# Optimization experiments

Measured on AMD Instinct MI355X. Metric: run time of the kernel, lower is better.

Reference implementation:

```python
import jax, jax.numpy as jnp
import numpy as np

B, S, IN, D, H, L, DFF, C = 64, 256, 32, 512, 8, 2, 2048, 16
DH = D // H


def setup_inputs() -> dict:
    key = jax.random.key(0)
    ks = iter(jax.random.split(key, 40))
    r = lambda shp, s=0.02: (jax.random.normal(next(ks), shp, dtype=jnp.float32) * s)
    inp = {
        'x': jax.random.normal(next(ks), (B, S, IN), dtype=jnp.float32),
        'W_emb': r((IN, D)), 'b_emb': jnp.zeros((D,), jnp.float32),
        'Wq': r((L, D, D)), 'bq': jnp.zeros((L, D), jnp.float32),
        'Wk': r((L, D, D)), 'bk': jnp.zeros((L, D), jnp.float32),
        'Wv': r((L, D, D)), 'bv': jnp.zeros((L, D), jnp.float32),
        'Wo': r((L, D, D)), 'bo': jnp.zeros((L, D), jnp.float32),
        'ln1_s': jnp.ones((L, D), jnp.float32), 'ln1_b': jnp.zeros((L, D), jnp.float32),
        'W1': r((L, D, DFF)), 'b1': jnp.zeros((L, DFF), jnp.float32),
        'W2': r((L, DFF, D)), 'b2': jnp.zeros((L, D), jnp.float32),
        'ln2_s': jnp.ones((L, D), jnp.float32), 'ln2_b': jnp.zeros((L, D), jnp.float32),
        'e1_w': r((D, 128)), 'e1_b': jnp.zeros((128,), jnp.float32),
        'e2_w': r((128, D)), 'e2_b': jnp.zeros((D,), jnp.float32),
        'd1_w': r((D, 128)), 'd1_b': jnp.zeros((128,), jnp.float32),
        'd2_w': r((128, D)), 'd2_b': jnp.zeros((D,), jnp.float32),
        'y': jax.random.randint(next(ks), (B, S, 1), 0, C, dtype=jnp.int32),
    }
    return inp


def _ln(x, s, b):
    m = x.mean(-1, keepdims=True)
    v = ((x - m) ** 2).mean(-1, keepdims=True)
    return (x - m) / jnp.sqrt(v + 1e-5) * s + b


def _ari(a, t, n_cls):
    # adjusted rand index from contingency matrix (labels in [0, n_cls))
    idx = a * n_cls + t
    cm = jnp.zeros((n_cls * n_cls,), jnp.float32).at[idx].add(1.0).reshape(n_cls, n_cls)
    comb2 = lambda m: m * (m - 1.0) * 0.5
    sij = comb2(cm).sum()
    sa = comb2(cm.sum(1)).sum()
    sb = comb2(cm.sum(0)).sum()
    n = jnp.float32(a.shape[0])
    exp = sa * sb / (n * (n - 1.0) * 0.5)
    mx = 0.5 * (sa + sb)
    return (sij - exp) / (mx - exp)


def _net(x, W_emb, b_emb, Wq, bq, Wk, bk, Wv, bv, Wo, bo, ln1_s, ln1_b,
         W1, b1, W2, b2, ln2_s, ln2_b, e1_w, e1_b, e2_w, e2_b, d1_w, d1_b, d2_w, d2_b):
    h = x @ W_emb + b_emb  # [B,S,D]
    for l in range(L):
        q = (h @ Wq[l] + bq[l]).reshape(B, S, H, DH)
        k = (h @ Wk[l] + bk[l]).reshape(B, S, H, DH)
        v = (h @ Wv[l] + bv[l]).reshape(B, S, H, DH)
        scores = jnp.einsum('bqhd,bkhd->bhqk', q, k) / jnp.sqrt(jnp.float32(DH))
        attn = jax.nn.softmax(scores, axis=-1)
        o = jnp.einsum('bhqk,bkhd->bqhd', attn, v).reshape(B, S, D)
        h = _ln(h + o @ Wo[l] + bo[l], ln1_s[l], ln1_b[l])
        f = jax.nn.relu(h @ W1[l] + b1[l]) @ W2[l] + b2[l]
        h = _ln(h + f, ln2_s[l], ln2_b[l])
    enc = jax.nn.relu(h @ e1_w + e1_b) @ e2_w + e2_b
    z = jax.nn.relu(enc @ d1_w + d1_b) @ d2_w + d2_b  # input_to_cluster [B,S,D]
    return z


def reference(x, W_emb, b_emb, Wq, bq, Wk, bk, Wv, bv, Wo, bo, ln1_s, ln1_b,
              W1, b1, W2, b2, ln2_s, ln2_b, e1_w, e1_b, e2_w, e2_b,
              d1_w, d1_b, d2_w, d2_b, y):
    z = _net(x, W_emb, b_emb, Wq, bq, Wk, bk, Wv, bv, Wo, bo, ln1_s, ln1_b,
             W1, b1, W2, b2, ln2_s, ln2_b, e1_w, e1_b, e2_w, e2_b, d1_w, d1_b, d2_w, d2_b)
    # pairwise squared distances across batch per timestep: [S,B,B]
    sq = jnp.sum(z * z, -1)                       # [B,S]
    gram = jnp.einsum('bsd,csd->sbc', z, z)       # [S,B,B]
    dist = sq.T[:, :, None] + sq.T[:, None, :] - 2.0 * gram
    p = jax.nn.softmax(-dist, axis=-1)
    _, knn = jax.lax.top_k(p, C)                  # [S,B,C]
    # tot_sum: rows of dist selected once per i where knn[s,b,i]==i
    counts = jnp.sum(knn == jnp.arange(C)[None, None, :], axis=-1)  # [S,B]
    tot_sum = jnp.sum(dist.sum(-1) * counts.astype(dist.dtype))
    # gather neighbor labels and take mode (ties -> smallest value, like torch.mode)
    y2 = y[..., 0]                                 # [B,S]
    labels = y2[knn, jnp.arange(S)[:, None, None]] # [S,B,C]
    cnt = jnp.sum(labels[..., None] == jnp.arange(C), axis=-2)      # [S,B,C]
    assigned = jnp.argmax(cnt, axis=-1).astype(jnp.int32).reshape(-1)  # S*B (row-major, as torch)
    y_true = y.reshape(-1)                         # B*S (as torch: mismatched order is faithful)
    ari = _ari(assigned, y_true, C)
    return tot_sum, ari, assigned, z
```

## Files before the change

### kernel.cpp

```cpp
#include <hip/hip_runtime.h>
#include <cstdint>
#include <cmath>

#define B_ 64
#define S_ 256
#define IN_ 32
#define D_ 512
#define H_ 8
#define L_ 2
#define DFF_ 2048
#define C_ 16
#define DH_ 64
#define NTOK (B_*S_)
#define HALF_ 8192

typedef __attribute__((ext_vector_type(8))) short bf16x8;
typedef __attribute__((ext_vector_type(4))) float f32x4;
typedef __attribute__((ext_vector_type(8))) ushort ushortx8;

__device__ __forceinline__ ushort bf16_rn(float x) {
    union { float f; uint32_t u; } v; v.f = x;
    uint32_t r = v.u + 0x7fffu + ((v.u >> 16) & 1u);
    return (ushort)(r >> 16);
}
__device__ __forceinline__ float bf16_f32(ushort h) {
    union { uint32_t u; float f; } v; v.u = ((uint32_t)h) << 16;
    return v.f;
}

#define GLDS(gp, lp) __builtin_amdgcn_global_load_lds( \
    (const __attribute__((address_space(1))) void*)(gp), \
    (__attribute__((address_space(3))) void*)(lp), 16, 0, 0)

__device__ __forceinline__ int xcd_swz(int lid, int nwg) {
    return (lid & 7) * (nwg >> 3) + (lid >> 3);
}

template<int MODE>
__global__ __launch_bounds__(256)
void gemm3(const ushort* __restrict__ Ahi, const ushort* __restrict__ Alo,
           const ushort* __restrict__ Bhi, const ushort* __restrict__ Blo,
           const float* __restrict__ bias,
           float* __restrict__ Cf, ushort* __restrict__ Chi, ushort* __restrict__ Clo,
           int M, int N, int K)
{
    __shared__ __align__(16) ushort Als[2][2][128*32];
    __shared__ __align__(16) ushort Bls[2][2][128*32];
    const int tid  = threadIdx.x;
    const int wave = tid >> 6, lane = tid & 63;
    const int nwg = gridDim.x * gridDim.y;
    const int swz = xcd_swz(blockIdx.y * gridDim.x + blockIdx.x, nwg);
    const int m0 = (swz / gridDim.x) << 7, n0 = (swz % gridDim.x) << 7;
    const int wr = wave >> 1, wc = wave & 1;

    const ushort* Ah = Ahi + (size_t)m0 * K;
    const ushort* Al = Alo + (size_t)m0 * K;
    const ushort* Bh = Bhi + (size_t)n0 * K;
    const ushort* Bl = Blo + (size_t)n0 * K;

    const int KT = K >> 5;

    f32x4 acc[4][4];
    #pragma unroll
    for (int m = 0; m < 4; ++m)
        #pragma unroll
        for (int n = 0; n < 4; ++n)
            acc[m][n] = (f32x4){0.f, 0.f, 0.f, 0.f};

    auto stage = [&](int buf, int kk) {
        #pragma unroll
        for (int i = 0; i < 2; ++i) {
            const int rbase = wave * 32 + i * 16;
            const int row   = rbase + (lane >> 2);
            const int slot  = (lane & 3) ^ ((row >> 1) & 3);
            GLDS(Ah + (size_t)row * K + kk + slot * 8, &Als[buf][0][rbase * 32]);
            GLDS(Al + (size_t)row * K + kk + slot * 8, &Als[buf][1][rbase * 32]);
            GLDS(Bh + (size_t)row * K + kk + slot * 8, &Bls[buf][0][rbase * 32]);
            GLDS(Bl + (size_t)row * K + kk + slot * 8, &Bls[buf][1][rbase * 32]);
        }
    };

    stage(0, 0);
    for (int t = 0; t < KT; ++t) {
        const int buf = t & 1;
        __syncthreads();
        if (t + 1 < KT) stage(buf ^ 1, (t + 1) << 5);

        const int chunk = lane >> 4;
        bf16x8 afh[4], afl[4], bfh[4], bfl[4];
        #pragma unroll
        for (int m = 0; m < 4; ++m) {
            const int row = wr * 64 + m * 16 + (lane & 15);
            const int sl  = chunk ^ ((row >> 1) & 3);
            afh[m] = *(const bf16x8*)(&Als[buf][0][row * 32 + sl * 8]);
            afl[m] = *(const bf16x8*)(&Als[buf][1][row * 32 + sl * 8]);
        }
        #pragma unroll
        for (int n = 0; n < 4; ++n) {
            const int row = wc * 64 + n * 16 + (lane & 15);
            const int sl  = chunk ^ ((row >> 1) & 3);
            bfh[n] = *(const bf16x8*)(&Bls[buf][0][row * 32 + sl * 8]);
            bfl[n] = *(const bf16x8*)(&Bls[buf][1][row * 32 + sl * 8]);
        }
        #pragma unroll
        for (int m = 0; m < 4; ++m)
            #pragma unroll
            for (int n = 0; n < 4; ++n) {
                acc[m][n] = __builtin_amdgcn_mfma_f32_16x16x32_bf16(afh[m], bfh[n], acc[m][n], 0, 0, 0);
                acc[m][n] = __builtin_amdgcn_mfma_f32_16x16x32_bf16(afh[m], bfl[n], acc[m][n], 0, 0, 0);
                acc[m][n] = __builtin_amdgcn_mfma_f32_16x16x32_bf16(afl[m], bfh[n], acc[m][n], 0, 0, 0);
            }
        __syncthreads();
    }

    const int col_l = lane & 15;
    float bv[4];
    #pragma unroll
    for (int n = 0; n < 4; ++n) bv[n] = bias[n0 + wc * 64 + n * 16 + col_l];
    #pragma unroll
    for (int m = 0; m < 4; ++m) {
        #pragma unroll
        for (int j = 0; j < 4; ++j) {
            const size_t grow = (size_t)(m0 + wr * 64 + m * 16 + (lane >> 4) * 4 + j);
            #pragma unroll
            for (int n = 0; n < 4; ++n) {
                float x = acc[m][n][j] + bv[n];
                if (MODE & 1) x = fmaxf(x, 0.f);
                const size_t gidx = grow * N + (n0 + wc * 64 + n * 16 + col_l);
                if (MODE < 2) {
                    Cf[gidx] = x;
                } else {
                    ushort hb = bf16_rn(x);
                    Chi[gidx] = hb;
                    Clo[gidx] = bf16_rn(x - bf16_f32(hb));
                }
            }
        }
    }
}

__global__ __launch_bounds__(256)
void qk_gemm(const ushort* __restrict__ qkvhi, const ushort* __restrict__ qkvlo,
             float* __restrict__ S)
{
    __shared__ __align__(16) ushort Als[2][2][128*32];
    __shared__ __align__(16) ushort Bls[2][2][128*32];
    const int tid = threadIdx.x, wave = tid >> 6, lane = tid & 63;
    const int swz = xcd_swz(blockIdx.y * 4 + blockIdx.x, 512);
    const int bh = swz >> 2;
    const int qt = (swz >> 1) & 1, kt = swz & 1;
    const int b = bh >> 3, h = bh & 7;
    const ushort* Ah = qkvhi + ((size_t)(b * 256 + qt * 128)) * 1536 + h * 64;
    const ushort* Al = qkvlo + ((size_t)(b * 256 + qt * 128)) * 1536 + h * 64;
    const ushort* Bh = qkvhi + ((size_t)(b * 256 + kt * 128)) * 1536 + 512 + h * 64;
    const ushort* Bl = qkvlo + ((size_t)(b * 256 + kt * 128)) * 1536 + 512 + h * 64;
    const int wr = wave >> 1, wc = wave & 1;

    f32x4 acc[4][4];
    #pragma unroll
    for (int m = 0; m < 4; ++m)
        #pragma unroll
        for (int n = 0; n < 4; ++n)
            acc[m][n] = (f32x4){0.f, 0.f, 0.f, 0.f};

    auto stage = [&](int buf, int kk) {
        #pragma unroll
        for (int i = 0; i < 2; ++i) {
            const int rbase = wave * 32 + i * 16;
            const int row   = rbase + (lane >> 2);
            const int slot  = (lane & 3) ^ ((row >> 1) & 3);
            GLDS(Ah + (size_t)row * 1536 + kk + slot * 8, &Als[buf][0][rbase * 32]);
            GLDS(Al + (size_t)row * 1536 + kk + slot * 8, &Als[buf][1][rbase * 32]);
            GLDS(Bh + (size_t)row * 1536 + kk + slot * 8, &Bls[buf][0][rbase * 32]);
            GLDS(Bl + (size_t)row * 1536 + kk + slot * 8, &Bls[buf][1][rbase * 32]);
        }
    };

    stage(0, 0);
    #pragma unroll
    for (int t = 0; t < 2; ++t) {
        __syncthreads();
        if (t == 0) stage(1, 32);
        const int chunk = lane >> 4;
        bf16x8 afh[4], afl[4], bfh[4], bfl[4];
        #pragma unroll
        for (int m = 0; m < 4; ++m) {
            const int row = wr * 64 + m * 16 + (lane & 15);
            const int sl  = chunk ^ ((row >> 1) & 3);
            afh[m] = *(const bf16x8*)(&Als[t][0][row * 32 + sl * 8]);
            afl[m] = *(const bf16x8*)(&Als[t][1][row * 32 + sl * 8]);
        }
        #pragma unroll
        for (int n = 0; n < 4; ++n) {
            const int row = wc * 64 + n * 16 + (lane & 15);
            const int sl  = chunk ^ ((row >> 1) & 3);
            bfh[n] = *(const bf16x8*)(&Bls[t][0][row * 32 + sl * 8]);
            bfl[n] = *(const bf16x8*)(&Bls[t][1][row * 32 + sl * 8]);
        }
        #pragma unroll
        for (int m = 0; m < 4; ++m)
            #pragma unroll
            for (int n = 0; n < 4; ++n) {
                acc[m][n] = __builtin_amdgcn_mfma_f32_16x16x32_bf16(afh[m], bfh[n], acc[m][n], 0, 0, 0);
                acc[m][n] = __builtin_amdgcn_mfma_f32_16x16x32_bf16(afh[m], bfl[n], acc[m][n], 0, 0, 0);
                acc[m][n] = __builtin_amdgcn_mfma_f32_16x16x32_bf16(afl[m], bfh[n], acc[m][n], 0, 0, 0);
            }
        __syncthreads();
    }

    const int col_l = lane & 15;
    #pragma unroll
    for (int m = 0; m < 4; ++m)
        #pragma unroll
        for (int j = 0; j < 4; ++j) {
            const int row = qt * 128 + wr * 64 + m * 16 + (lane >> 4) * 4 + j;
            #pragma unroll
            for (int n = 0; n < 4; ++n) {
                const int col = kt * 128 + wc * 64 + n * 16 + col_l;
                S[(size_t)bh * 65536 + (size_t)row * 256 + col] = acc[m][n][j] * 0.125f;
            }
        }
}

__global__ __launch_bounds__(256)
void softmax_p(const float* __restrict__ S, ushort* __restrict__ Phi,
               ushort* __restrict__ Plo)
{
    const int row = blockIdx.x * 4 + (threadIdx.x >> 6);
    const int lane = threadIdx.x & 63;
    float4 v = *(const float4*)(S + (size_t)row * 256 + lane * 4);
    float mx = fmaxf(fmaxf(v.x, v.y), fmaxf(v.z, v.w));
    #pragma unroll
    for (int d = 1; d < 64; d <<= 1) mx = fmaxf(mx, __shfl_xor(mx, d));
    float e0 = expf(v.x - mx), e1 = expf(v.y - mx);
    float e2 = expf(v.z - mx), e3 = expf(v.w - mx);
    float s = (e0 + e1) + (e2 + e3);
    #pragma unroll
    for (int d = 1; d < 64; d <<= 1) s += __shfl_xor(s, d);
    const float inv = 1.0f / s;
    float p0 = e0 * inv, p1 = e1 * inv, p2 = e2 * inv, p3 = e3 * inv;
    ushort4 hh, ll;
    hh.x = bf16_rn(p0); ll.x = bf16_rn(p0 - bf16_f32(hh.x));
    hh.y = bf16_rn(p1); ll.y = bf16_rn(p1 - bf16_f32(hh.y));
    hh.z = bf16_rn(p2); ll.z = bf16_rn(p2 - bf16_f32(hh.z));
    hh.w = bf16_rn(p3); ll.w = bf16_rn(p3 - bf16_f32(hh.w));
    *(ushort4*)(Phi + (size_t)row * 256 + lane * 4) = hh;
    *(ushort4*)(Plo + (size_t)row * 256 + lane * 4) = ll;
}

__global__ __launch_bounds__(256)
void vtrans(const ushort* __restrict__ qkvhi, const ushort* __restrict__ qkvlo,
            ushort* __restrict__ VThi, ushort* __restrict__ VTlo)
{
    __shared__ ushort T[64][272];
    const int bh = blockIdx.x;
    const int b = bh >> 3, h = bh & 7;
    const int tid = threadIdx.x;
    #pragma unroll
    for (int pass = 0; pass < 2; ++pass) {
        const ushort* src = pass ? qkvlo : qkvhi;
        ushort* dst = pass ? VTlo : VThi;
        const ushort* p = src + ((size_t)b * 256 + tid) * 1536 + 1024 + h * 64;
        #pragma unroll
        for (int i = 0; i < 8; ++i) {
            ushortx8 v = *(const ushortx8*)(p + i * 8);
            #pragma unroll
            for (int j = 0; j < 8; ++j) T[i * 8 + j][tid] = v[j];
        }
        __syncthreads();
        const int dh = tid >> 2, k0 = (tid & 3) * 64;
        ushort* op = dst + ((size_t)bh * 64 + dh) * 256 + k0;
        #pragma unroll
        for (int i = 0; i < 8; ++i)
            *(ushortx8*)(op + i * 8) = *(const ushortx8*)&T[dh][k0 + i * 8];
        __syncthreads();
    }
}

__global__ __launch_bounds__(256)
void pv_gemm(const ushort* __restrict__ Phi, const ushort* __restrict__ Plo,
             const ushort* __restrict__ VThi, const ushort* __restrict__ VTlo,
             ushort* __restrict__ obhi, ushort* __restrict__ oblo, int t0)
{
    __shared__ __align__(16) ushort Als[2][2][128*32];
    __shared__ __align__(16) ushort Bls[2][2][64*32];
    const int tid = threadIdx.x, wave = tid >> 6, lane = tid & 63;
    const int swz = xcd_swz(blockIdx.y * 2 + blockIdx.x, 256);
    const int bh = swz >> 1, qt = swz & 1;
    const ushort* Ah = Phi + ((size_t)bh * 256 + qt * 128) * 256;
    const ushort* Al = Plo + ((size_t)bh * 256 + qt * 128) * 256;
    const ushort* Bh = VThi + (size_t)bh * 64 * 256;
    const ushort* Bl = VTlo + (size_t)bh * 64 * 256;

    f32x4 acc[2][4];
    #pragma unroll
    for (int m = 0; m < 2; ++m)
        #pragma unroll
        for (int n = 0; n < 4; ++n)
            acc[m][n] = (f32x4){0.f, 0.f, 0.f, 0.f};

    auto stage = [&](int buf, int kk) {
        #pragma unroll
        for (int i = 0; i < 2; ++i) {
            const int rbase = wave * 32 + i * 16;
            const int row   = rbase + (lane >> 2);
            const int slot  = (lane & 3) ^ ((row >> 1) & 3);
            GLDS(Ah + (size_t)row * 256 + kk + slot * 8, &Als[buf][0][rbase * 32]);
            GLDS(Al + (size_t)row * 256 + kk + slot * 8, &Als[buf][1][rbase * 32]);
        }
        const int rbase2 = wave * 16;
        const int row2   = rbase2 + (lane >> 2);
        const int slot2  = (lane & 3) ^ ((row2 >> 1) & 3);
        GLDS(Bh + (size_t)row2 * 256 + kk + slot2 * 8, &Bls[buf][0][rbase2 * 32]);
        GLDS(Bl + (size_t)row2 * 256 + kk + slot2 * 8, &Bls[buf][1][rbase2 * 32]);
    };

    stage(0, 0);
    for (int t = 0; t < 8; ++t) {
        const int buf = t & 1;
        __syncthreads();
        if (t < 7) stage(buf ^ 1, (t + 1) << 5);
        const int chunk = lane >> 4;
        bf16x8 afh[2], afl[2], bfh[4], bfl[4];
        #pragma unroll
        for (int m = 0; m < 2; ++m) {
            const int row = wave * 32 + m * 16 + (lane & 15);
            const int sl  = chunk ^ ((row >> 1) & 3);
            afh[m] = *(const bf16x8*)(&Als[buf][0][row * 32 + sl * 8]);
            afl[m] = *(const bf16x8*)(&Als[buf][1][row * 32 + sl * 8]);
        }
        #pragma unroll
        for (int n = 0; n < 4; ++n) {
            const int row = n * 16 + (lane & 15);
            const int sl  = chunk ^ ((row >> 1) & 3);
            bfh[n] = *(const bf16x8*)(&Bls[buf][0][row * 32 + sl * 8]);
            bfl[n] = *(const bf16x8*)(&Bls[buf][1][row * 32 + sl * 8]);
        }
        #pragma unroll
        for (int m = 0; m < 2; ++m)
            #pragma unroll
            for (int n = 0; n < 4; ++n) {
                acc[m][n] = __builtin_amdgcn_mfma_f32_16x16x32_bf16(afh[m], bfh[n], acc[m][n], 0, 0, 0);
                acc[m][n] = __builtin_amdgcn_mfma_f32_16x16x32_bf16(afh[m], bfl[n], acc[m][n], 0, 0, 0);
                acc[m][n] = __builtin_amdgcn_mfma_f32_16x16x32_bf16(afl[m], bfh[n], acc[m][n], 0, 0, 0);
            }
        __syncthreads();
    }

    const int b = bh >> 3, h = bh & 7;
    const int col_l = lane & 15;
    #pragma unroll
    for (int m = 0; m < 2; ++m)
        #pragma unroll
        for (int j = 0; j < 4; ++j) {
            const int q = qt * 128 + wave * 32 + m * 16 + (lane >> 4) * 4 + j;
            const size_t token = (size_t)t0 + (size_t)b * 256 + q;
            #pragma unroll
            for (int n = 0; n < 4; ++n) {
                const int col = h * 64 + n * 16 + col_l;
                float x = acc[m][n][j];
                ushort hb = bf16_rn(x);
                obhi[token * 512 + col] = hb;
                oblo[token * 512 + col] = bf16_rn(x - bf16_f32(hb));
            }
        }
}

__global__ __launch_bounds__(256)
void gemm_f32(const float* __restrict__ A, const float* __restrict__ W,
              const float* __restrict__ bias, float* __restrict__ Cc,
              ushort* __restrict__ Chi, ushort* __restrict__ Clo,
              int M, int N, int K)
{
    __shared__ float As[16][68];
    __shared__ float Bs[16][64];
    const int tid = threadIdx.x;
    const int tx = tid & 15, ty = tid >> 4;
    const int m0 = blockIdx.y << 6, n0 = blockIdx.x << 6;
    const int arow = tid >> 2, ak4 = (tid & 3) << 2;
    const int brow = tid >> 4, bc4 = (tid & 15) << 2;
    float acc[4][4] = {};
    const float* aptr = A + (size_t)(m0 + arow) * K + ak4;
    const float* bptr = W + (size_t)brow * N + n0 + bc4;
    for (int k0 = 0; k0 < K; k0 += 16) {
        float4 av = *(const float4*)(aptr + k0);
        float4 bv = *(const float4*)(bptr + (size_t)k0 * N);
        __syncthreads();
        As[ak4+0][arow] = av.x; As[ak4+1][arow] = av.y;
        As[ak4+2][arow] = av.z; As[ak4+3][arow] = av.w;
        *(float4*)&Bs[brow][bc4] = bv;
        __syncthreads();
        #pragma unroll
        for (int kk = 0; kk < 16; ++kk) {
            float4 a = *(const float4*)&As[kk][ty << 2];
            float4 b = *(const float4*)&Bs[kk][tx << 2];
            float ar[4] = {a.x,a.y,a.z,a.w};
            float br[4] = {b.x,b.y,b.z,b.w};
            #pragma unroll
            for (int i = 0; i < 4; ++i)
                #pragma unroll
                for (int j = 0; j < 4; ++j)
                    acc[i][j] = fmaf(ar[i], br[j], acc[i][j]);
        }
    }
    float4 bb = *(const float4*)(bias + n0 + (tx << 2));
    #pragma unroll
    for (int i = 0; i < 4; ++i) {
        int m = m0 + (ty << 2) + i;
        float o[4];
        o[0] = acc[i][0] + bb.x; o[1] = acc[i][1] + bb.y;
        o[2] = acc[i][2] + bb.z; o[3] = acc[i][3] + bb.w;
        ushort4 hh, ll;
        hh.x = bf16_rn(o[0]); ll.x = bf16_rn(o[0] - bf16_f32(hh.x));
        hh.y = bf16_rn(o[1]); ll.y = bf16_rn(o[1] - bf16_f32(hh.y));
        hh.z = bf16_rn(o[2]); ll.z = bf16_rn(o[2] - bf16_f32(hh.z));
        hh.w = bf16_rn(o[3]); ll.w = bf16_rn(o[3] - bf16_f32(hh.w));
        const size_t base = (size_t)m * N + n0 + (tx << 2);
        *(float4*)(Cc + base) = (float4){o[0],o[1],o[2],o[3]};
        *(ushort4*)(Chi + base) = hh;
        *(ushort4*)(Clo + base) = ll;
    }
}

__global__ __launch_bounds__(256)
void transpose_split(const float* __restrict__ W, ushort* __restrict__ Thi,
                     ushort* __restrict__ Tlo, int K, int N)
{
    __shared__ float T[64][65];
    const int k0 = blockIdx.y << 6, n0 = blockIdx.x << 6;
    const int tid = threadIdx.x;
    #pragma unroll
    for (int i = 0; i < 16; ++i) {
        int idx = tid + i * 256;
        int kl = idx >> 6, nl = idx & 63;
        T[nl][kl] = W[(size_t)(k0 + kl) * N + n0 + nl];
    }
    __syncthreads();
    #pragma unroll
    for (int i = 0; i < 16; ++i) {
        int idx = tid + i * 256;
        int nl = idx >> 6, kl = idx & 63;
        float x = T[nl][kl];
        ushort hb = bf16_rn(x);
        size_t o = (size_t)(n0 + nl) * K + k0 + kl;
        Thi[o] = hb;
        Tlo[o] = bf16_rn(x - bf16_f32(hb));
    }
}

__global__ __launch_bounds__(256)
void concat3(const float* __restrict__ a, const float* __restrict__ b,
             const float* __restrict__ c, float* __restrict__ out)
{
    int i = blockIdx.x * 256 + threadIdx.x;
    out[i] = (i < 512) ? a[i] : (i < 1024 ? b[i - 512] : c[i - 1024]);
}

__global__ __launch_bounds__(64)
void ln_res(float* __restrict__ h, const float* __restrict__ t,
            const float* __restrict__ sc, const float* __restrict__ bi,
            ushort* __restrict__ hhi, ushort* __restrict__ hlo)
{
    const int row = blockIdx.x, lane = threadIdx.x;
    const size_t off = (size_t)row * D_ + (size_t)lane * 8;
    float x[8];
    float4 a0 = *(const float4*)(h + off),  a1 = *(const float4*)(h + off + 4);
    float4 b0 = *(const float4*)(t + off),  b1 = *(const float4*)(t + off + 4);
    x[0]=a0.x+b0.x; x[1]=a0.y+b0.y; x[2]=a0.z+b0.z; x[3]=a0.w+b0.w;
    x[4]=a1.x+b1.x; x[5]=a1.y+b1.y; x[6]=a1.z+b1.z; x[7]=a1.w+b1.w;

    float s = 0.f;
    #pragma unroll
    for (int i = 0; i < 8; ++i) s += x[i];
    #pragma unroll
    for (int d = 1; d < 64; d <<= 1) s += __shfl_xor(s, d);
    float mean = s * (1.0f / 512.0f);

    float vsum = 0.f;
    #pragma unroll
    for (int i = 0; i < 8; ++i) { float dx = x[i] - mean; vsum += dx * dx; }
    #pragma unroll
    for (int d = 1; d < 64; d <<= 1) vsum += __shfl_xor(vsum, d);
    float den = sqrtf(vsum * (1.0f / 512.0f) + 1e-5f);

    float4 s0 = *(const float4*)(sc + lane*8), s1 = *(const float4*)(sc + lane*8 + 4);
    float4 c0 = *(const float4*)(bi + lane*8), c1 = *(const float4*)(bi + lane*8 + 4);
    float scv[8] = {s0.x,s0.y,s0.z,s0.w,s1.x,s1.y,s1.z,s1.w};
    float biv[8] = {c0.x,c0.y,c0.z,c0.w,c1.x,c1.y,c1.z,c1.w};
    float out[8];
    ushort hh[8], ll[8];
    #pragma unroll
    for (int i = 0; i < 8; ++i) {
        out[i] = (x[i] - mean) / den * scv[i] + biv[i];
        hh[i] = bf16_rn(out[i]);
        ll[i] = bf16_rn(out[i] - bf16_f32(hh[i]));
    }
    *(float4*)(h + off)     = (float4){out[0],out[1],out[2],out[3]};
    *(float4*)(h + off + 4) = (float4){out[4],out[5],out[6],out[7]};
    *(ushort4*)(hhi + off)     = (ushort4){hh[0],hh[1],hh[2],hh[3]};
    *(ushort4*)(hhi + off + 4) = (ushort4){hh[4],hh[5],hh[6],hh[7]};
    *(ushort4*)(hlo + off)     = (ushort4){ll[0],ll[1],ll[2],ll[3]};
    *(ushort4*)(hlo + off + 4) = (ushort4){ll[4],ll[5],ll[6],ll[7]};
}

__global__ __launch_bounds__(64)
void sq_kernel(const float* __restrict__ z, float* __restrict__ sq)
{
#pragma clang fp contract(off)
    const int row = blockIdx.x, lane = threadIdx.x;
    const float* p = z + (size_t)row * D_ + (size_t)lane * 8;
    float4 a0 = *(const float4*)(p), a1 = *(const float4*)(p + 4);
    float s = 0.f;
    float vv[8] = {a0.x,a0.y,a0.z,a0.w,a1.x,a1.y,a1.z,a1.w};
    #pragma unroll
    for (int i = 0; i < 8; ++i) { float t = vv[i] * vv[i]; s = s + t; }
    #pragma unroll
    for (int d = 1; d < 64; d <<= 1) s += __shfl_xor(s, d);
    if (lane == 0) sq[row] = s;
}

__global__ __launch_bounds__(256)
void copy_z(const float* __restrict__ z, float* __restrict__ out)
{
    size_t i4 = (size_t)blockIdx.x * 256 + threadIdx.x;
    if (i4 < (size_t)NTOK * D_ / 4) {
        float4 t = ((const float4*)z)[i4];
        out[i4*4+0] = t.x; out[i4*4+1] = t.y;
        out[i4*4+2] = t.z; out[i4*4+3] = t.w;
    }
}

__global__ __launch_bounds__(256)
void gram_kernel(const float* __restrict__ z, float* __restrict__ gram)
{
    __shared__ float Ls[16][68];
    const int s = blockIdx.x;
    const int tid = threadIdx.x;
    const int tx = tid & 15, ty = tid >> 4;
    const int arow = tid >> 2, ak4 = (tid & 3) << 2;
    float acc[4][4] = {};
    const float* zp = z + ((size_t)arow * S_ + s) * D_ + ak4;
    for (int k0 = 0; k0 < D_; k0 += 16) {
        float4 av = *(const float4*)(zp + k0);
        __syncthreads();
        Ls[ak4+0][arow] = av.x; Ls[ak4+1][arow] = av.y;
        Ls[ak4+2][arow] = av.z; Ls[ak4+3][arow] = av.w;
        __syncthreads();
        #pragma unroll
        for (int kk = 0; kk < 16; ++kk) {
            float4 a = *(const float4*)&Ls[kk][ty << 2];
            float4 b = *(const float4*)&Ls[kk][tx << 2];
            float ar[4] = {a.x,a.y,a.z,a.w};
            float br[4] = {b.x,b.y,b.z,b.w};
            #pragma unroll
            for (int i = 0; i < 4; ++i)
                #pragma unroll
                for (int j = 0; j < 4; ++j)
                    acc[i][j] = fmaf(ar[i], br[j], acc[i][j]);
        }
    }
    #pragma unroll
    for (int i = 0; i < 4; ++i) {
        float4 o = {acc[i][0], acc[i][1], acc[i][2], acc[i][3]};
        *(float4*)(gram + ((size_t)s * 64 + (ty<<2) + i) * 64 + (tx<<2)) = o;
    }
}

__global__ __launch_bounds__(64)
void cluster_kernel(const float* __restrict__ gram, const float* __restrict__ sq,
                    const int* __restrict__ y, float* __restrict__ contrib,
                    int* __restrict__ assigned, float* __restrict__ out_assigned_f)
{
#pragma clang fp contract(off)
    __shared__ float G[64][65];
    __shared__ float sqs[64];
    const int s = blockIdx.x, b = threadIdx.x;
    for (int i = b; i < 4096; i += 64)
        G[i >> 6][i & 63] = gram[(size_t)s * 4096 + i];
    sqs[b] = sq[(size_t)b * S_ + s];
    __syncthreads();

    const float sqb = sqs[b];
    float dmin = INFINITY, dsum = 0.f;
    for (int c = 0; c < 64; ++c) {
        float d = sqb + sqs[c] - 2.0f * G[b][c];
        dmin = fminf(dmin, d);
        dsum = dsum + d;
    }
    float Z = 0.f;
    for (int c = 0; c < 64; ++c) {
        float d = sqb + sqs[c] - 2.0f * G[b][c];
        float e = expf(dmin - d);
        G[b][c] = e;
        Z = Z + e;
    }
    for (int c = 0; c < 64; ++c) G[b][c] = G[b][c] / Z;

    int knn[16];
    #pragma unroll
    for (int j = 0; j < 16; ++j) {
        float bp = -1.f; int bi2 = 0;
        for (int c = 0; c < 64; ++c) {
            float pv = G[b][c];
            if (pv > bp) { bp = pv; bi2 = c; }
        }
        knn[j] = bi2;
        G[b][bi2] = -1.f;
    }
    int cmatch = 0;
    #pragma unroll
    for (int j = 0; j < 16; ++j) cmatch += (knn[j] == j) ? 1 : 0;
    int lab[16];
    #pragma unroll
    for (int j = 0; j < 16; ++j) lab[j] = y[knn[j] * S_ + s];
    int bestc = -1, bestcls = 0;
    #pragma unroll
    for (int cls = 0; cls < 16; ++cls) {
        int cc = 0;
        #pragma unroll
        for (int j = 0; j < 16; ++j) cc += (lab[j] == cls) ? 1 : 0;
        if (cc > bestc) { bestc = cc; bestcls = cls; }
    }
    const int oi = s * 64 + b;
    contrib[oi] = dsum * (float)cmatch;
    assigned[oi] = bestcls;
    out_assigned_f[oi] = (float)bestcls;
}

__global__ __launch_bounds__(256)
void finalize_kernel(const float* __restrict__ contrib, const int* __restrict__ assigned,
                     const int* __restrict__ y, float* __restrict__ dout)
{
#pragma clang fp contract(off)
    __shared__ int cm[256];
    __shared__ float red[256];
    const int tid = threadIdx.x;
    cm[tid] = 0;
    float s = 0.f;
    for (int i = tid; i < NTOK; i += 256) s = s + contrib[i];
    red[tid] = s;
    __syncthreads();
    for (int i = tid; i < NTOK; i += 256)
        atomicAdd(&cm[assigned[i] * 16 + y[i]], 1);
    __syncthreads();
    for (int st = 128; st > 0; st >>= 1) {
        if (tid < st) red[tid] = red[tid] + red[tid + st];
        __syncthreads();
    }
    if (tid == 0) {
        dout[0] = red[0];
        float sij = 0.f, sa = 0.f, sb = 0.f;
        for (int i = 0; i < 256; ++i) {
            float mm = (float)cm[i];
            sij = sij + mm * (mm - 1.0f) * 0.5f;
        }
        for (int r = 0; r < 16; ++r) {
            int rs = 0;
            for (int c2 = 0; c2 < 16; ++c2) rs += cm[r * 16 + c2];
            float mm = (float)rs;
            sa = sa + mm * (mm - 1.0f) * 0.5f;
        }
        for (int c2 = 0; c2 < 16; ++c2) {
            int cs = 0;
            for (int r = 0; r < 16; ++r) cs += cm[r * 16 + c2];
            float mm = (float)cs;
            sb = sb + mm * (mm - 1.0f) * 0.5f;
        }
        float n = 16384.0f;
        float expv = sa * sb / (n * (n - 1.0f) * 0.5f);
        float mx = 0.5f * (sa + sb);
        dout[1] = (sij - expv) / (mx - expv);
    }
}

extern "C" void kernel_launch(void* const* d_in, const int* in_sizes, int n_in,
                              void* d_out, int out_size, void* d_ws, size_t ws_size,
                              hipStream_t stream)
{
    (void)in_sizes; (void)n_in; (void)out_size; (void)ws_size;
    const float* x     = (const float*)d_in[0];
    const float* W_emb = (const float*)d_in[1];
    const float* b_emb = (const float*)d_in[2];
    const float* Wq    = (const float*)d_in[3];
    const float* bq    = (const float*)d_in[4];
    const float* Wk    = (const float*)d_in[5];
    const float* bk    = (const float*)d_in[6];
    const float* Wv    = (const float*)d_in[7];
    const float* bv    = (const float*)d_in[8];
    const float* Wo    = (const float*)d_in[9];
    const float* bo    = (const float*)d_in[10];
    const float* ln1_s = (const float*)d_in[11];
    const float* ln1_b = (const float*)d_in[12];
    const float* W1    = (const float*)d_in[13];
    const float* b1    = (const float*)d_in[14];
    const float* W2    = (const float*)d_in[15];
    const float* b2    = (const float*)d_in[16];
    const float* ln2_s = (const float*)d_in[17];
    const float* ln2_b = (const float*)d_in[18];
    const float* e1_w  = (const float*)d_in[19];
    const float* e1_b  = (const float*)d_in[20];
    const float* e2_w  = (const float*)d_in[21];
    const float* e2_b  = (const float*)d_in[22];
    const float* d1_w  = (const float*)d_in[23];
    const float* d1_b  = (const float*)d_in[24];
    const float* d2_w  = (const float*)d_in[25];
    const float* d2_b  = (const float*)d_in[26];
    const int*   y     = (const int*)d_in[27];

    float* ws = (float*)d_ws;
    float*  h    = ws;
    ushort* hhi  = (ushort*)(ws + 8388608);
    ushort* hlo  = (ushort*)(ws + 12582912);
    float*  SCR  = ws + 16777216;
    ushort* obhi = (ushort*)(ws + 37748736);
    ushort* oblo = (ushort*)(ws + 41943040);
    float*  wt   = ws + 46137344;
    ushort* WTQKV_HI = (ushort*)wt;
    ushort* WTQKV_LO = WTQKV_HI + 786432;
    ushort* WTO_HI   = WTQKV_LO + 786432;
    ushort* WTO_LO   = WTO_HI + 262144;
    ushort* WT1_HI   = WTO_LO + 262144;
    ushort* WT1_LO   = WT1_HI + 1048576;
    ushort* WT2_HI   = WT1_LO + 1048576;
    ushort* WT2_LO   = WT2_HI + 1048576;
    ushort* WE1_HI   = WT2_LO + 1048576;
    ushort* WE1_LO   = WE1_HI + 65536;
    ushort* WE2_HI   = WE1_LO + 65536;
    ushort* WE2_LO   = WE2_HI + 65536;
    ushort* WD1_HI   = WE2_LO + 65536;
    ushort* WD1_LO   = WD1_HI + 65536;
    ushort* WD2_HI   = WD1_LO + 65536;
    ushort* WD2_LO   = WD2_HI + 65536;
    float*  biasqkv  = ws + 49545216;

    float*  Sb    = SCR;
    ushort* qkvhi = (ushort*)(SCR + 8388608);
    ushort* qkvlo = (ushort*)(SCR + 11534336);
    ushort* VThi  = (ushort*)(SCR + 14680064);
    ushort* VTlo  = (ushort*)(SCR + 15728640);
    ushort* Phi_  = (ushort*)(SCR + 8388608);
    ushort* Plo_  = (ushort*)(SCR + 16777216);
    float*  Of32  = SCR;
    ushort* f1hi  = (ushort*)SCR;
    ushort* f1lo  = (ushort*)(SCR + 8388608);
    float*  Xhalf = SCR + 16777216;
    ushort* enchi = (ushort*)SCR;
    ushort* enclo = (ushort*)(SCR + 4194304);
    float*  z     = SCR + 8388608;
    float*  gram  = SCR + 16777216;
    float*  sqb_  = SCR + 17825792;
    float*  contrib = SCR + 17842176;
    int*    assigned = (int*)(SCR + 17858560);
    ushort* t1hi = obhi;
    ushort* t1lo = oblo;
    ushort* t2hi = obhi + 2097152;
    ushort* t2lo = oblo + 2097152;
    float*  dout = (float*)d_out;

    dim3 blk(256);
    auto gg = [](int M, int N) { return dim3(N >> 7, M >> 7); };

    transpose_split<<<dim3(2, 8), blk, 0, stream>>>(e1_w, WE1_HI, WE1_LO, 512, 128);
    transpose_split<<<dim3(8, 2), blk, 0, stream>>>(e2_w, WE2_HI, WE2_LO, 128, 512);
    transpose_split<<<dim3(2, 8), blk, 0, stream>>>(d1_w, WD1_HI, WD1_LO, 512, 128);
    transpose_split<<<dim3(8, 2), blk, 0, stream>>>(d2_w, WD2_HI, WD2_LO, 128, 512);

    gemm_f32<<<dim3(8, 256), blk, 0, stream>>>(x, W_emb, b_emb, h, hhi, hlo, NTOK, D_, IN_);

    for (int l = 0; l < L_; ++l) {
        transpose_split<<<dim3(8, 8), blk, 0, stream>>>(Wq + (size_t)l*D_*D_, WTQKV_HI,            WTQKV_LO,            512, 512);
        transpose_split<<<dim3(8, 8), blk, 0, stream>>>(Wk + (size_t)l*D_*D_, WTQKV_HI + 512*512,  WTQKV_LO + 512*512,  512, 512);
        transpose_split<<<dim3(8, 8), blk, 0, stream>>>(Wv + (size_t)l*D_*D_, WTQKV_HI + 1024*512, WTQKV_LO + 1024*512, 512, 512);
        transpose_split<<<dim3(8, 8), blk, 0, stream>>>(Wo + (size_t)l*D_*D_, WTO_HI, WTO_LO, 512, 512);
        transpose_split<<<dim3(32, 8), blk, 0, stream>>>(W1 + (size_t)l*D_*DFF_, WT1_HI, WT1_LO, 512, 2048);
        transpose_split<<<dim3(8, 32), blk, 0, stream>>>(W2 + (size_t)l*DFF_*D_, WT2_HI, WT2_LO, 2048, 512);
        concat3<<<dim3(6), blk, 0, stream>>>(bq + l*D_, bk + l*D_, bv + l*D_, biasqkv);

        for (int qtr = 0; qtr < 4; ++qtr) {
            const size_t hoff = (size_t)qtr * 4096 * 512;
            gemm3<2><<<gg(4096, 1536), blk, 0, stream>>>(
                hhi + hoff, hlo + hoff, WTQKV_HI, WTQKV_LO, biasqkv,
                nullptr, qkvhi, qkvlo, 4096, 1536, 512);
            vtrans<<<dim3(128), blk, 0, stream>>>(qkvhi, qkvlo, VThi, VTlo);
            qk_gemm<<<dim3(4, 128), blk, 0, stream>>>(qkvhi, qkvlo, Sb);
            softmax_p<<<dim3(8192), blk, 0, stream>>>(Sb, Phi_, Plo_);
            pv_gemm<<<dim3(2, 128), blk, 0, stream>>>(Phi_, Plo_, VThi, VTlo,
                                                      obhi, oblo, qtr * 4096);
        }
        gemm3<0><<<gg(NTOK, 512), blk, 0, stream>>>(
            obhi, oblo, WTO_HI, WTO_LO, bo + l*D_,
            Of32, nullptr, nullptr, NTOK, 512, 512);
        ln_res<<<dim3(NTOK), dim3(64), 0, stream>>>(h, Of32, ln1_s + l*D_, ln1_b + l*D_, hhi, hlo);

        for (int half = 0; half < 2; ++half) {
            const size_t ro = (size_t)half * HALF_ * D_;
            gemm3<3><<<gg(HALF_, DFF_), blk, 0, stream>>>(
                hhi + ro, hlo + ro, WT1_HI, WT1_LO, b1 + l*DFF_,
                nullptr, f1hi, f1lo, HALF_, 2048, 512);
            gemm3<0><<<gg(HALF_, 512), blk, 0, stream>>>(
                f1hi, f1lo, WT2_HI, WT2_LO, b2 + l*D_,
                Xhalf, nullptr, nullptr, HALF_, 512, 2048);
            ln_res<<<dim3(HALF_), dim3(64), 0, stream>>>(
                h + ro, Xhalf, ln2_s + l*D_, ln2_b + l*D_, hhi + ro, hlo + ro);
        }
    }

    gemm3<3><<<gg(NTOK, 128), blk, 0, stream>>>(
        hhi, hlo, WE1_HI, WE1_LO, e1_b, nullptr, t1hi, t1lo, NTOK, 128, 512);
    gemm3<2><<<gg(NTOK, 512), blk, 0, stream>>>(
        t1hi, t1lo, WE2_HI, WE2_LO, e2_b, nullptr, enchi, enclo, NTOK, 512, 128);
    gemm3<3><<<gg(NTOK, 128), blk, 0, stream>>>(
        enchi, enclo, WD1_HI, WD1_LO, d1_b, nullptr, t2hi, t2lo, NTOK, 128, 512);
    gemm3<0><<<gg(NTOK, 512), blk, 0, stream>>>(
        t2hi, t2lo, WD2_HI, WD2_LO, d2_b, z, nullptr, nullptr, NTOK, 512, 128);

    copy_z<<<dim3(NTOK * D_ / 4 / 256), blk, 0, stream>>>(z, dout + 16386);
    sq_kernel<<<dim3(NTOK), dim3(64), 0, stream>>>(z, sqb_);
    gram_kernel<<<dim3(S_), blk, 0, stream>>>(z, gram);
    cluster_kernel<<<dim3(S_), dim3(64), 0, stream>>>(gram, sqb_, y, contrib, assigned, dout + 2);
    finalize_kernel<<<dim3(1), blk, 0, stream>>>(contrib, assigned, y, dout);
}
```

Baseline: 1.565 ms.

## Split bf16x3 GEMM into sequential hi/lo K-segments to halve LDS and registers

The split-bf16 GEMM used to stage hi and lo halves of A and B together and issue three MFMAs per fragment pair. It now loops three times over K, once each for hi*hi, hi*lo and lo*hi, staging only one A and one B tile per step. LDS use and fragment registers are halved, and launch bounds ask for 4 blocks per CU to raise occupancy. In exchange the hi operands are read from global memory twice, there are three times as many barrier-separated iterations, and the sum order changes slightly.

```diff
diff --git a/kernel.cpp b/kernel.cpp
--- a/kernel.cpp
+++ b/kernel.cpp
@@ -37,15 +37,15 @@
 }
 
 template<int MODE>
-__global__ __launch_bounds__(256)
+__global__ __launch_bounds__(256, 4)
 void gemm3(const ushort* __restrict__ Ahi, const ushort* __restrict__ Alo,
            const ushort* __restrict__ Bhi, const ushort* __restrict__ Blo,
            const float* __restrict__ bias,
            float* __restrict__ Cf, ushort* __restrict__ Chi, ushort* __restrict__ Clo,
            int M, int N, int K)
 {
-    __shared__ __align__(16) ushort Als[2][2][128*32];
-    __shared__ __align__(16) ushort Bls[2][2][128*32];
+    __shared__ __align__(16) ushort Als[2][128*32];
+    __shared__ __align__(16) ushort Bls[2][128*32];
     const int tid  = threadIdx.x;
     const int wave = tid >> 6, lane = tid & 63;
     const int nwg = gridDim.x * gridDim.y;
@@ -53,12 +53,11 @@
     const int m0 = (swz / gridDim.x) << 7, n0 = (swz % gridDim.x) << 7;
     const int wr = wave >> 1, wc = wave & 1;
 
-    const ushort* Ah = Ahi + (size_t)m0 * K;
-    const ushort* Al = Alo + (size_t)m0 * K;
-    const ushort* Bh = Bhi + (size_t)n0 * K;
-    const ushort* Bl = Blo + (size_t)n0 * K;
+    const ushort* Aseg[3] = { Ahi + (size_t)m0 * K, Ahi + (size_t)m0 * K, Alo + (size_t)m0 * K };
+    const ushort* Bseg[3] = { Bhi + (size_t)n0 * K, Blo + (size_t)n0 * K, Bhi + (size_t)n0 * K };
 
     const int KT = K >> 5;
+    const int NT = 3 * KT;
 
     f32x4 acc[4][4];
     #pragma unroll
@@ -67,50 +66,47 @@
         for (int n = 0; n < 4; ++n)
             acc[m][n] = (f32x4){0.f, 0.f, 0.f, 0.f};
 
-    auto stage = [&](int buf, int kk) {
+    auto stage = [&](int buf, const ushort* As, const ushort* Bs, int kk) {
         #pragma unroll
         for (int i = 0; i < 2; ++i) {
             const int rbase = wave * 32 + i * 16;
             const int row   = rbase + (lane >> 2);
             const int slot  = (lane & 3) ^ ((row >> 1) & 3);
-            GLDS(Ah + (size_t)row * K + kk + slot * 8, &Als[buf][0][rbase * 32]);
-            GLDS(Al + (size_t)row * K + kk + slot * 8, &Als[buf][1][rbase * 32]);
-            GLDS(Bh + (size_t)row * K + kk + slot * 8, &Bls[buf][0][rbase * 32]);
-            GLDS(Bl + (size_t)row * K + kk + slot * 8, &Bls[buf][1][rbase * 32]);
+            GLDS(As + (size_t)row * K + kk + slot * 8, &Als[buf][rbase * 32]);
+            GLDS(Bs + (size_t)row * K + kk + slot * 8, &Bls[buf][rbase * 32]);
         }
     };
 
-    stage(0, 0);
-    for (int t = 0; t < KT; ++t) {
+    int seg = 0, kt = 0;
+    stage(0, Aseg[0], Bseg[0], 0);
+    for (int t = 0; t < NT; ++t) {
         const int buf = t & 1;
-        __syncthreads();
-        if (t + 1 < KT) stage(buf ^ 1, (t + 1) << 5);
-
+        int nseg = seg, nkt = kt + 1;
+        if (nkt == KT) { nkt = 0; nseg = seg + 1; }
+        __syncthreads();
+        if (t + 1 < NT) stage(buf ^ 1, Aseg[nseg], Bseg[nseg], nkt << 5);
+
+        bf16x8 af[4], bfr[4];
         const int chunk = lane >> 4;
-        bf16x8 afh[4], afl[4], bfh[4], bfl[4];
         #pragma unroll
         for (int m = 0; m < 4; ++m) {
             const int row = wr * 64 + m * 16 + (lane & 15);
             const int sl  = chunk ^ ((row >> 1) & 3);
-            afh[m] = *(const bf16x8*)(&Als[buf][0][row * 32 + sl * 8]);
-            afl[m] = *(const bf16x8*)(&Als[buf][1][row * 32 + sl * 8]);
+            af[m] = *(const bf16x8*)(&Als[buf][row * 32 + sl * 8]);
         }
         #pragma unroll
         for (int n = 0; n < 4; ++n) {
             const int row = wc * 64 + n * 16 + (lane & 15);
             const int sl  = chunk ^ ((row >> 1) & 3);
-            bfh[n] = *(const bf16x8*)(&Bls[buf][0][row * 32 + sl * 8]);
-            bfl[n] = *(const bf16x8*)(&Bls[buf][1][row * 32 + sl * 8]);
+            bfr[n] = *(const bf16x8*)(&Bls[buf][row * 32 + sl * 8]);
         }
         #pragma unroll
         for (int m = 0; m < 4; ++m)
             #pragma unroll
-            for (int n = 0; n < 4; ++n) {
-                acc[m][n] = __builtin_amdgcn_mfma_f32_16x16x32_bf16(afh[m], bfh[n], acc[m][n], 0, 0, 0);
-                acc[m][n] = __builtin_amdgcn_mfma_f32_16x16x32_bf16(afh[m], bfl[n], acc[m][n], 0, 0, 0);
-                acc[m][n] = __builtin_amdgcn_mfma_f32_16x16x32_bf16(afl[m], bfh[n], acc[m][n], 0, 0, 0);
-            }
-        __syncthreads();
+            for (int n = 0; n < 4; ++n)
+                acc[m][n] = __builtin_amdgcn_mfma_f32_16x16x32_bf16(af[m], bfr[n], acc[m][n], 0, 0, 0);
+        __syncthreads();
+        seg = nseg; kt = nkt;
     }
 
     const int col_l = lane & 15;
```

Result: slower. 1.859 ms (+18.7%).
